# Kernel optimization log

Measured on AMD Instinct MI355X. Metric: run time of the kernel, lower is better.

## Reference

```python
import jax, jax.numpy as jnp
import numpy as np

B, C, D = 8, 512, 128

def setup_inputs() -> dict:
    key = jax.random.key(0)
    k1, k2, k3 = jax.random.split(key, 3)
    queries = jax.random.normal(k1, (B, C, D), dtype=jnp.float32)
    keys = jax.random.normal(k2, (B, C, D), dtype=jnp.float32)
    # docstring says keys are L2-normalized
    keys = keys / jnp.linalg.norm(keys, axis=-1, keepdims=True)
    carry_over = jax.random.normal(k3, (D, D), dtype=jnp.float32) * 0.1
    return {"queries": queries, "keys": keys, "carry_over": carry_over}

def reference(queries, keys, carry_over):
    # per-position outer products: (B, C, D, D)
    outer = jnp.einsum('bci,bcj->bcij', keys, keys)
    # causal prefix-sum state + carried-over state from previous chunk
    proj = jnp.cumsum(outer, axis=1) + carry_over[None, None, :, :]
    # apply state to queries: out_i = sum_j proj[b,c,i,j] * q[b,c,j]
    projected_queries = jnp.einsum('bcij,bcj->bci', proj, queries)
    # new carry: batch-mean of final-position state
    new_carry_over = jnp.mean(proj[:, -1], axis=0)
    return projected_queries, new_carry_over
```

## Files before the change

### kernel.cpp

```cpp
#include <hip/hip_runtime.h>

#define B_ 8
#define C_ 512
#define D_ 128
#define LDK 136
#define LDT 40

typedef __bf16 v8bf __attribute__((ext_vector_type(8)));
typedef float v4f __attribute__((ext_vector_type(4)));
typedef float fvec4 __attribute__((ext_vector_type(4)));
typedef unsigned short u16;
typedef u16 u16x4 __attribute__((ext_vector_type(4)));

__device__ __forceinline__ u16 f2bf(float f) {
  unsigned u = __builtin_bit_cast(unsigned, f);
  u = u + 0x7FFFu + ((u >> 16) & 1u);
  return (u16)(u >> 16);
}

__global__ __launch_bounds__(256) void k_gram(const float* __restrict__ K,
                                              float* __restrict__ G) {
  const int t = blockIdx.x, b = blockIdx.y;
  const int tid = threadIdx.x;
  const int w = tid >> 6, l = tid & 63, lr = l & 15, lg = l >> 4;
  const float* Kc = K + (size_t)(b * C_ + t * 32) * D_;

  v8bf fr[8];
#pragma unroll
  for (int n = 0; n < 8; ++n) {
    u16 tmp[8];
#pragma unroll
    for (int e = 0; e < 8; ++e)
      tmp[e] = f2bf(Kc[(size_t)(8 * lg + e) * D_ + 16 * n + lr]);
    fr[n] = *(const v8bf*)tmp;
  }
  float* Gp = G + (size_t)(b * 16 + t) * 16384;
#pragma unroll
  for (int mi = 0; mi < 2; ++mi) {
    v8bf am = fr[2 * w + mi];
#pragma unroll
    for (int n = 0; n < 8; ++n) {
      v4f z = {0.f, 0.f, 0.f, 0.f};
      v4f a = __builtin_amdgcn_mfma_f32_16x16x32_bf16(am, fr[n], z, 0, 0, 0);
#pragma unroll
      for (int j = 0; j < 4; ++j)
        Gp[(size_t)(32 * w + 16 * mi + 4 * lg + j) * 128 + 16 * n + lr] = a[j];
    }
  }
}

__global__ __launch_bounds__(256) void k_prefix(const float* __restrict__ G,
                                                const float* __restrict__ carry,
                                                u16* __restrict__ Mp,
                                                float* __restrict__ tot) {
  const int b = blockIdx.y;
  const int e = blockIdx.x * 256 + threadIdx.x;
  const float c = carry[e];
  const float* gb = G + (size_t)b * 16 * 16384 + e;
  u16* mb = Mp + (size_t)b * 16 * 16384 + e;
  float run = 0.f;
#pragma unroll
  for (int t = 0; t < 16; ++t) {
    float g = gb[(size_t)t * 16384];
    mb[(size_t)t * 16384] = f2bf(c + run);
    run += g;
  }
  tot[(size_t)b * 16384 + e] = run;
}

__global__ __launch_bounds__(256) void k_out(
    const float* __restrict__ Q, const float* __restrict__ K,
    const u16* __restrict__ Mp, const float* __restrict__ tot,
    const float* __restrict__ carry, float* __restrict__ out,
    float* __restrict__ out2) {
  const int t = blockIdx.x, b = blockIdx.y;
  const int tid = threadIdx.x;

  if (t == 16) {
    const int e0 = b * 2048 + tid * 8;
    fvec4 s0 = {0.f, 0.f, 0.f, 0.f}, s1 = {0.f, 0.f, 0.f, 0.f};
#pragma unroll
    for (int bb = 0; bb < 8; ++bb) {
      s0 += *(const fvec4*)(tot + (size_t)bb * 16384 + e0);
      s1 += *(const fvec4*)(tot + (size_t)bb * 16384 + e0 + 4);
    }
    fvec4 c0 = *(const fvec4*)(carry + e0);
    fvec4 c1 = *(const fvec4*)(carry + e0 + 4);
    *(fvec4*)(out2 + e0) = c0 + 0.125f * s0;
    *(fvec4*)(out2 + e0 + 4) = c1 + 0.125f * s1;
    return;
  }

  const int w = tid >> 6, l = tid & 63, lr = l & 15, lg = l >> 4;
  const int wr = (w & 1) * 16, wc = (w >> 1) * 64, sc0 = (w >> 1) * 16;
  const int r0 = t * 32;

  __shared__ u16 sl[32 * 40];

  const float* Kc = K + (size_t)(b * C_ + r0) * D_;

  v8bf pb[4];
#pragma unroll
  for (int n = 0; n < 4; ++n) {
    u16 tmp[8];
#pragma unroll
    for (int e = 0; e < 8; ++e)
      tmp[e] = f2bf(Kc[(size_t)(8 * lg + e) * D_ + wc + 16 * n + lr]);
    pb[n] = *(const v8bf*)tmp;
  }

  v8bf sb[4];
  {
    const float* krow = Kc + (size_t)(sc0 + lr) * D_;
#pragma unroll
    for (int kk = 0; kk < 4; ++kk) {
      fvec4 a = *(const fvec4*)(krow + kk * 32 + 8 * lg);
      fvec4 c2 = *(const fvec4*)(krow + kk * 32 + 8 * lg + 4);
      u16 tmp[8] = {f2bf(a[0]),  f2bf(a[1]),  f2bf(a[2]),  f2bf(a[3]),
                    f2bf(c2[0]), f2bf(c2[1]), f2bf(c2[2]), f2bf(c2[3])};
      sb[kk] = *(const v8bf*)tmp;
    }
  }

  v8bf qf[4];
  {
    const float* qrow = Q + (size_t)(b * C_ + r0 + wr + lr) * D_;
#pragma unroll
    for (int kk = 0; kk < 4; ++kk) {
      const float* p = qrow + kk * 32 + 8 * lg;
      fvec4 a = *(const fvec4*)p;
      fvec4 c2 = *(const fvec4*)(p + 4);
      u16 tmp[8] = {f2bf(a[0]),  f2bf(a[1]),  f2bf(a[2]),  f2bf(a[3]),
                    f2bf(c2[0]), f2bf(c2[1]), f2bf(c2[2]), f2bf(c2[3])};
      qf[kk] = *(const v8bf*)tmp;
    }
  }

  v8bf mf[4][4];
  {
    const u16* mp = Mp + (size_t)(b * 16 + t) * 16384;
#pragma unroll
    for (int kk = 0; kk < 4; ++kk)
#pragma unroll
      for (int n = 0; n < 4; ++n)
        mf[kk][n] =
            *(const v8bf*)(mp + (size_t)(wc + 16 * n + lr) * 128 + 32 * kk +
                           8 * lg);
  }

  v4f sacc = {0.f, 0.f, 0.f, 0.f};
#pragma unroll
  for (int kk = 0; kk < 4; ++kk)
    sacc = __builtin_amdgcn_mfma_f32_16x16x32_bf16(qf[kk], sb[kk], sacc, 0, 0, 0);
#pragma unroll
  for (int j = 0; j < 4; ++j) {
    const int sr = wr + lg * 4 + j;
    const int sc = sc0 + lr;
    float v = sacc[j];
    if (sc > sr) v = 0.f;
    sl[sr * 40 + sc] = f2bf(v);
  }

  v4f acc[4] = {{0.f, 0.f, 0.f, 0.f}, {0.f, 0.f, 0.f, 0.f},
                {0.f, 0.f, 0.f, 0.f}, {0.f, 0.f, 0.f, 0.f}};
#pragma unroll
  for (int kk = 0; kk < 4; ++kk)
#pragma unroll
    for (int n = 0; n < 4; ++n)
      acc[n] = __builtin_amdgcn_mfma_f32_16x16x32_bf16(qf[kk], mf[kk][n],
                                                       acc[n], 0, 0, 0);
  __syncthreads();

  v8bf af = *(const v8bf*)&sl[(wr + lr) * 40 + lg * 8];
#pragma unroll
  for (int n = 0; n < 4; ++n)
    acc[n] = __builtin_amdgcn_mfma_f32_16x16x32_bf16(af, pb[n], acc[n], 0, 0, 0);

#pragma unroll
  for (int n = 0; n < 4; ++n)
#pragma unroll
    for (int j = 0; j < 4; ++j)
      out[(size_t)(b * C_ + r0 + wr + lg * 4 + j) * D_ + wc + n * 16 + lr] =
          acc[n][j];
}

__device__ __forceinline__ int kt_idx(int d, int r) {
  return d * LDT + ((((r >> 3) ^ ((d >> 2) & 3))) << 3) + (r & 7);
}
__device__ __forceinline__ v8bf kt_frag(const u16* ktb, int col, int lg) {
  return *(const v8bf*)&ktb[col * LDT + (((lg ^ ((col >> 2) & 3))) << 3)];
}
__device__ __forceinline__ void load_chunk(const float* __restrict__ Kbase,
                                           int tid, fvec4* pf) {
#pragma unroll
  for (int i = 0; i < 4; ++i)
    pf[i] = *(const fvec4*)(Kbase + i * 1024 + tid * 4);
}
__device__ __forceinline__ void write_stage(const fvec4* pf, u16* ksb, u16* ktb,
                                            int tid) {
  const int d0 = (tid & 31) * 4;
  const int rb = tid >> 5;
#pragma unroll
  for (int i = 0; i < 4; ++i) {
    const int r = i * 8 + rb;
    fvec4 v = pf[i];
    u16 h0 = f2bf(v[0]), h1 = f2bf(v[1]), h2 = f2bf(v[2]), h3 = f2bf(v[3]);
    u16x4 u = {h0, h1, h2, h3};
    *(u16x4*)&ksb[r * LDK + d0] = u;
    ktb[kt_idx(d0 + 0, r)] = h0;
    ktb[kt_idx(d0 + 1, r)] = h1;
    ktb[kt_idx(d0 + 2, r)] = h2;
    ktb[kt_idx(d0 + 3, r)] = h3;
  }
}

__global__ __launch_bounds__(256) void k_proj_fb(
    const float* __restrict__ Q, const float* __restrict__ K,
    const float* __restrict__ carry, float* __restrict__ out) {
  const int t = blockIdx.x, b = blockIdx.y;
  const int tid = threadIdx.x;
  const int w = tid >> 6, l = tid & 63, lr = l & 15, lg = l >> 4;
  const int wr = (w & 1) * 16, wc = (w >> 1) * 64;
  const int r0 = t * 32;

  __shared__ u16 ks[2][32 * LDK];
  __shared__ u16 kt[2][128 * LDT];
  __shared__ u16 sl[32 * 40];

  const float* Kb0 = K + (size_t)(b * C_) * D_;
  fvec4 pf[4];
  load_chunk(Kb0, tid, pf);

  v8bf qf[4];
  {
    const float* qrow = Q + (size_t)(b * C_ + r0 + wr + lr) * D_;
#pragma unroll
    for (int kk = 0; kk < 4; ++kk) {
      const float* p = qrow + kk * 32 + lg * 8;
      fvec4 a = *(const fvec4*)p;
      fvec4 c2 = *(const fvec4*)(p + 4);
      u16 tmp[8] = {f2bf(a[0]),  f2bf(a[1]),  f2bf(a[2]),  f2bf(a[3]),
                    f2bf(c2[0]), f2bf(c2[1]), f2bf(c2[2]), f2bf(c2[3])};
      qf[kk] = *(const v8bf*)tmp;
    }
  }

  v4f acc[4] = {{0.f, 0.f, 0.f, 0.f}, {0.f, 0.f, 0.f, 0.f},
                {0.f, 0.f, 0.f, 0.f}, {0.f, 0.f, 0.f, 0.f}};
#pragma unroll
  for (int kk = 0; kk < 4; ++kk) {
#pragma unroll
    for (int n = 0; n < 4; ++n) {
      const float* p =
          carry + (size_t)(wc + n * 16 + lr) * D_ + kk * 32 + lg * 8;
      fvec4 a = *(const fvec4*)p;
      fvec4 c2 = *(const fvec4*)(p + 4);
      u16 tmp[8] = {f2bf(a[0]),  f2bf(a[1]),  f2bf(a[2]),  f2bf(a[3]),
                    f2bf(c2[0]), f2bf(c2[1]), f2bf(c2[2]), f2bf(c2[3])};
      acc[n] = __builtin_amdgcn_mfma_f32_16x16x32_bf16(
          qf[kk], *(const v8bf*)tmp, acc[n], 0, 0, 0);
    }
  }

  write_stage(pf, ks[0], kt[0], tid);
  __syncthreads();

  int cur = 0;
  const int sc0 = (w >> 1) * 16;
  for (int cc = 0; cc <= t; ++cc) {
    const bool more = (cc < t);
    fvec4 nf[4];
    if (more) load_chunk(Kb0 + (size_t)(cc + 1) * 32 * D_, tid, nf);

    v4f sacc = {0.f, 0.f, 0.f, 0.f};
#pragma unroll
    for (int kk = 0; kk < 4; ++kk) {
      v8bf bf = *(const v8bf*)&ks[cur][(sc0 + lr) * LDK + kk * 32 + lg * 8];
      sacc = __builtin_amdgcn_mfma_f32_16x16x32_bf16(qf[kk], bf, sacc, 0, 0, 0);
    }
    const bool diag = (cc == t);
#pragma unroll
    for (int j = 0; j < 4; ++j) {
      const int sr = wr + lg * 4 + j;
      const int sc = sc0 + lr;
      float v = sacc[j];
      if (diag && sc > sr) v = 0.f;
      sl[sr * 40 + sc] = f2bf(v);
    }
    __syncthreads();

    v8bf af = *(const v8bf*)&sl[(wr + lr) * 40 + lg * 8];
#pragma unroll
    for (int n = 0; n < 4; ++n) {
      v8bf bf = kt_frag(kt[cur], wc + n * 16 + lr, lg);
      acc[n] = __builtin_amdgcn_mfma_f32_16x16x32_bf16(af, bf, acc[n], 0, 0, 0);
    }
    if (more) {
      write_stage(nf, ks[cur ^ 1], kt[cur ^ 1], tid);
      cur ^= 1;
    }
    __syncthreads();
  }

#pragma unroll
  for (int n = 0; n < 4; ++n)
#pragma unroll
    for (int j = 0; j < 4; ++j)
      out[(size_t)(b * C_ + r0 + wr + lg * 4 + j) * D_ + wc + n * 16 + lr] =
          acc[n][j];
}

__global__ __launch_bounds__(256) void k_syrk_direct(
    const float* __restrict__ K, const float* __restrict__ carry,
    float* __restrict__ out2) {
  const int tid = threadIdx.x;
  const int w = tid >> 6, l = tid & 63, lr = l & 15, lg = l >> 4;
  __shared__ u16 kt[2][128 * LDT];

  v4f acc[2][8];
#pragma unroll
  for (int mi = 0; mi < 2; ++mi)
#pragma unroll
    for (int n = 0; n < 8; ++n) acc[mi][n] = (v4f){0.f, 0.f, 0.f, 0.f};

  fvec4 pf[4];
  load_chunk(K, tid, pf);
  {
    const int d0 = (tid & 31) * 4;
    const int rb = tid >> 5;
#pragma unroll
    for (int i = 0; i < 4; ++i) {
      const int r = i * 8 + rb;
      fvec4 v = pf[i];
      kt[0][kt_idx(d0 + 0, r)] = f2bf(v[0]);
      kt[0][kt_idx(d0 + 1, r)] = f2bf(v[1]);
      kt[0][kt_idx(d0 + 2, r)] = f2bf(v[2]);
      kt[0][kt_idx(d0 + 3, r)] = f2bf(v[3]);
    }
  }
  __syncthreads();
  int cur = 0;
  for (int g = 0; g < 128; ++g) {
    const bool more = (g < 127);
    fvec4 nf[4];
    if (more) load_chunk(K + (size_t)(g + 1) * 32 * D_, tid, nf);
    v8bf fr[8];
#pragma unroll
    for (int x = 0; x < 8; ++x) fr[x] = kt_frag(kt[cur], x * 16 + lr, lg);
#pragma unroll
    for (int mi = 0; mi < 2; ++mi)
#pragma unroll
      for (int n = 0; n < 8; ++n)
        acc[mi][n] = __builtin_amdgcn_mfma_f32_16x16x32_bf16(
            fr[2 * w + mi], fr[n], acc[mi][n], 0, 0, 0);
    if (more) {
      const int d0 = (tid & 31) * 4;
      const int rb = tid >> 5;
      u16* kb = kt[cur ^ 1];
#pragma unroll
      for (int i = 0; i < 4; ++i) {
        const int r = i * 8 + rb;
        fvec4 v = nf[i];
        kb[kt_idx(d0 + 0, r)] = f2bf(v[0]);
        kb[kt_idx(d0 + 1, r)] = f2bf(v[1]);
        kb[kt_idx(d0 + 2, r)] = f2bf(v[2]);
        kb[kt_idx(d0 + 3, r)] = f2bf(v[3]);
      }
      cur ^= 1;
    }
    __syncthreads();
  }
#pragma unroll
  for (int mi = 0; mi < 2; ++mi)
#pragma unroll
    for (int n = 0; n < 8; ++n)
#pragma unroll
      for (int j = 0; j < 4; ++j) {
        const int idx = (16 * (2 * w + mi) + 4 * lg + j) * 128 + 16 * n + lr;
        out2[idx] = carry[idx] + 0.125f * acc[mi][n][j];
      }
}

extern "C" void kernel_launch(void* const* d_in, const int* in_sizes, int n_in,
                              void* d_out, int out_size, void* d_ws,
                              size_t ws_size, hipStream_t stream) {
  const float* Q = (const float*)d_in[0];
  const float* K = (const float*)d_in[1];
  const float* carry = (const float*)d_in[2];
  float* out = (float*)d_out;
  float* out2 = out + (size_t)B_ * C_ * D_;

  const size_t nG = (size_t)128 * 16384;
  const size_t nMpF = nG / 2;
  const size_t need = (nG + nMpF + (size_t)8 * 16384) * sizeof(float);

  if (ws_size >= need) {
    float* G = (float*)d_ws;
    u16* Mp = (u16*)((float*)d_ws + nG);
    float* tot = (float*)d_ws + nG + nMpF;
    k_gram<<<dim3(16, 8), 256, 0, stream>>>(K, G);
    k_prefix<<<dim3(64, 8), 256, 0, stream>>>(G, carry, Mp, tot);
    k_out<<<dim3(17, 8), 256, 0, stream>>>(Q, K, Mp, tot, carry, out, out2);
  } else {
    k_proj_fb<<<dim3(16, 8), 256, 0, stream>>>(Q, K, carry, out);
    k_syrk_direct<<<1, 256, 0, stream>>>(K, carry, out2);
  }
}
```

Baseline: 27.85 us.

## Drop prefix-scan kernel; accumulate prior chunk Grams directly in output kernel

Removes the separate k_prefix kernel. k_gram now stores per-chunk Gram matrices in bf16, and each k_out block loops over all earlier chunks' Grams with MFMA instead of reading a precomputed prefix state. The carry contribution is applied by converting carry to bf16 on the fly, and the new-carry block sums all 128 bf16 Grams itself. This saves one launch and the fp32 G round trip, but adds load imbalance (later chunks do up to 15x more MFMA work), a serial 128-step reduction in one block, and extra bf16 rounding error on the per-chunk sums.

Result: slower. 67.54 us (+142.5%).

```diff
diff --git a/kernel.cpp b/kernel.cpp
--- a/kernel.cpp
+++ b/kernel.cpp
@@ -11,15 +11,20 @@
 typedef float fvec4 __attribute__((ext_vector_type(4)));
 typedef unsigned short u16;
 typedef u16 u16x4 __attribute__((ext_vector_type(4)));
+typedef u16 u16x8 __attribute__((ext_vector_type(8)));
 
 __device__ __forceinline__ u16 f2bf(float f) {
   unsigned u = __builtin_bit_cast(unsigned, f);
   u = u + 0x7FFFu + ((u >> 16) & 1u);
   return (u16)(u >> 16);
 }
+__device__ __forceinline__ float bf2f(u16 h) {
+  unsigned u = ((unsigned)h) << 16;
+  return __builtin_bit_cast(float, u);
+}
 
 __global__ __launch_bounds__(256) void k_gram(const float* __restrict__ K,
-                                              float* __restrict__ G) {
+                                              u16* __restrict__ G) {
   const int t = blockIdx.x, b = blockIdx.y;
   const int tid = threadIdx.x;
   const int w = tid >> 6, l = tid & 63, lr = l & 15, lg = l >> 4;
@@ -34,7 +39,7 @@
       tmp[e] = f2bf(Kc[(size_t)(8 * lg + e) * D_ + 16 * n + lr]);
     fr[n] = *(const v8bf*)tmp;
   }
-  float* Gp = G + (size_t)(b * 16 + t) * 16384;
+  u16* Gp = G + (size_t)(b * 16 + t) * 16384;
 #pragma unroll
   for (int mi = 0; mi < 2; ++mi) {
     v8bf am = fr[2 * w + mi];
@@ -44,50 +49,30 @@
       v4f a = __builtin_amdgcn_mfma_f32_16x16x32_bf16(am, fr[n], z, 0, 0, 0);
 #pragma unroll
       for (int j = 0; j < 4; ++j)
-        Gp[(size_t)(32 * w + 16 * mi + 4 * lg + j) * 128 + 16 * n + lr] = a[j];
-    }
-  }
-}
-
-__global__ __launch_bounds__(256) void k_prefix(const float* __restrict__ G,
-                                                const float* __restrict__ carry,
-                                                u16* __restrict__ Mp,
-                                                float* __restrict__ tot) {
-  const int b = blockIdx.y;
-  const int e = blockIdx.x * 256 + threadIdx.x;
-  const float c = carry[e];
-  const float* gb = G + (size_t)b * 16 * 16384 + e;
-  u16* mb = Mp + (size_t)b * 16 * 16384 + e;
-  float run = 0.f;
-#pragma unroll
-  for (int t = 0; t < 16; ++t) {
-    float g = gb[(size_t)t * 16384];
-    mb[(size_t)t * 16384] = f2bf(c + run);
-    run += g;
-  }
-  tot[(size_t)b * 16384 + e] = run;
+        Gp[(size_t)(32 * w + 16 * mi + 4 * lg + j) * 128 + 16 * n + lr] =
+            f2bf(a[j]);
+    }
+  }
 }
 
 __global__ __launch_bounds__(256) void k_out(
     const float* __restrict__ Q, const float* __restrict__ K,
-    const u16* __restrict__ Mp, const float* __restrict__ tot,
-    const float* __restrict__ carry, float* __restrict__ out,
-    float* __restrict__ out2) {
+    const u16* __restrict__ G, const float* __restrict__ carry,
+    float* __restrict__ out, float* __restrict__ out2) {
   const int t = blockIdx.x, b = blockIdx.y;
   const int tid = threadIdx.x;
 
   if (t == 16) {
     const int e0 = b * 2048 + tid * 8;
-    fvec4 s0 = {0.f, 0.f, 0.f, 0.f}, s1 = {0.f, 0.f, 0.f, 0.f};
-#pragma unroll
-    for (int bb = 0; bb < 8; ++bb) {
-      s0 += *(const fvec4*)(tot + (size_t)bb * 16384 + e0);
-      s1 += *(const fvec4*)(tot + (size_t)bb * 16384 + e0 + 4);
-    }
-    fvec4 c0 = *(const fvec4*)(carry + e0);
-    fvec4 c1 = *(const fvec4*)(carry + e0 + 4);
-    *(fvec4*)(out2 + e0) = c0 + 0.125f * s0;
-    *(fvec4*)(out2 + e0 + 4) = c1 + 0.125f * s1;
+    float s[8] = {0.f, 0.f, 0.f, 0.f, 0.f, 0.f, 0.f, 0.f};
+    for (int p = 0; p < 128; ++p) {
+      u16x8 g = *(const u16x8*)(G + (size_t)p * 16384 + e0);
+#pragma unroll
+      for (int i = 0; i < 8; ++i) s[i] += bf2f(g[i]);
+    }
+#pragma unroll
+    for (int i = 0; i < 8; ++i)
+      out2[e0 + i] = carry[e0 + i] + 0.125f * s[i];
     return;
   }
 
@@ -136,22 +121,11 @@
     }
   }
 
-  v8bf mf[4][4];
-  {
-    const u16* mp = Mp + (size_t)(b * 16 + t) * 16384;
-#pragma unroll
-    for (int kk = 0; kk < 4; ++kk)
-#pragma unroll
-      for (int n = 0; n < 4; ++n)
-        mf[kk][n] =
-            *(const v8bf*)(mp + (size_t)(wc + 16 * n + lr) * 128 + 32 * kk +
-                           8 * lg);
-  }
-
   v4f sacc = {0.f, 0.f, 0.f, 0.f};
 #pragma unroll
   for (int kk = 0; kk < 4; ++kk)
-    sacc = __builtin_amdgcn_mfma_f32_16x16x32_bf16(qf[kk], sb[kk], sacc, 0, 0, 0);
+    sacc =
+        __builtin_amdgcn_mfma_f32_16x16x32_bf16(qf[kk], sb[kk], sacc, 0, 0, 0);
 #pragma unroll
   for (int j = 0; j < 4; ++j) {
     const int sr = wr + lg * 4 + j;
@@ -164,17 +138,41 @@
   v4f acc[4] = {{0.f, 0.f, 0.f, 0.f}, {0.f, 0.f, 0.f, 0.f},
                 {0.f, 0.f, 0.f, 0.f}, {0.f, 0.f, 0.f, 0.f}};
 #pragma unroll
-  for (int kk = 0; kk < 4; ++kk)
-#pragma unroll
-    for (int n = 0; n < 4; ++n)
-      acc[n] = __builtin_amdgcn_mfma_f32_16x16x32_bf16(qf[kk], mf[kk][n],
-                                                       acc[n], 0, 0, 0);
+  for (int kk = 0; kk < 4; ++kk) {
+#pragma unroll
+    for (int n = 0; n < 4; ++n) {
+      const float* p =
+          carry + (size_t)(wc + 16 * n + lr) * D_ + 32 * kk + 8 * lg;
+      fvec4 a = *(const fvec4*)p;
+      fvec4 c2 = *(const fvec4*)(p + 4);
+      u16 tmp[8] = {f2bf(a[0]),  f2bf(a[1]),  f2bf(a[2]),  f2bf(a[3]),
+                    f2bf(c2[0]), f2bf(c2[1]), f2bf(c2[2]), f2bf(c2[3])};
+      acc[n] = __builtin_amdgcn_mfma_f32_16x16x32_bf16(
+          qf[kk], *(const v8bf*)tmp, acc[n], 0, 0, 0);
+    }
+  }
+
+  const u16* Gb = G + (size_t)(b * 16) * 16384;
+  for (int tp = 0; tp < t; ++tp) {
+    const u16* gp = Gb + (size_t)tp * 16384;
+#pragma unroll
+    for (int kk = 0; kk < 4; ++kk) {
+#pragma unroll
+      for (int n = 0; n < 4; ++n) {
+        v8bf mf = *(const v8bf*)(gp + (size_t)(wc + 16 * n + lr) * 128 +
+                                 32 * kk + 8 * lg);
+        acc[n] = __builtin_amdgcn_mfma_f32_16x16x32_bf16(qf[kk], mf, acc[n],
+                                                         0, 0, 0);
+      }
+    }
+  }
   __syncthreads();
 
   v8bf af = *(const v8bf*)&sl[(wr + lr) * 40 + lg * 8];
 #pragma unroll
   for (int n = 0; n < 4; ++n)
-    acc[n] = __builtin_amdgcn_mfma_f32_16x16x32_bf16(af, pb[n], acc[n], 0, 0, 0);
+    acc[n] =
+        __builtin_amdgcn_mfma_f32_16x16x32_bf16(af, pb[n], acc[n], 0, 0, 0);
 
 #pragma unroll
   for (int n = 0; n < 4; ++n)
@@ -390,17 +388,12 @@
   float* out = (float*)d_out;
   float* out2 = out + (size_t)B_ * C_ * D_;
 
-  const size_t nG = (size_t)128 * 16384;
-  const size_t nMpF = nG / 2;
-  const size_t need = (nG + nMpF + (size_t)8 * 16384) * sizeof(float);
+  const size_t need = (size_t)128 * 16384 * sizeof(u16);
 
   if (ws_size >= need) {
-    float* G = (float*)d_ws;
-    u16* Mp = (u16*)((float*)d_ws + nG);
-    float* tot = (float*)d_ws + nG + nMpF;
+    u16* G = (u16*)d_ws;
     k_gram<<<dim3(16, 8), 256, 0, stream>>>(K, G);
-    k_prefix<<<dim3(64, 8), 256, 0, stream>>>(G, carry, Mp, tot);
-    k_out<<<dim3(17, 8), 256, 0, stream>>>(Q, K, Mp, tot, carry, out, out2);
+    k_out<<<dim3(17, 8), 256, 0, stream>>>(Q, K, G, carry, out, out2);
   } else {
     k_proj_fb<<<dim3(16, 8), 256, 0, stream>>>(Q, K, carry, out);
     k_syrk_direct<<<1, 256, 0, stream>>>(K, carry, out2);
```

## Store per-chunk Gram matrices in bf16 and stage K tiles through LDS

Applied to the files above, without the earlier changes.

The per-chunk Gram matrices are now written in bf16 instead of fp32, which halves the workspace traffic between the gram and prefix kernels. The prefix kernel processes eight elements per thread with vector loads and stores and launches far fewer blocks. The gram and output kernels now load K with coalesced vector reads into LDS and build MFMA fragments from there, replacing strided scalar global loads. The trade-off is extra bf16 rounding in the prefix-sum accumulation, which may reduce accuracy of the carried state.

After: 26.74 us. 4.0% less time.

```diff
diff --git a/kernel.cpp b/kernel.cpp
--- a/kernel.cpp
+++ b/kernel.cpp
@@ -3,6 +3,8 @@
 #define B_ 8
 #define C_ 512
 #define D_ 128
+#define LDG 132
+#define LDO 136
 #define LDK 136
 #define LDT 40
 
@@ -11,30 +13,60 @@
 typedef float fvec4 __attribute__((ext_vector_type(4)));
 typedef unsigned short u16;
 typedef u16 u16x4 __attribute__((ext_vector_type(4)));
+typedef u16 u16x8 __attribute__((ext_vector_type(8)));
 
 __device__ __forceinline__ u16 f2bf(float f) {
   unsigned u = __builtin_bit_cast(unsigned, f);
   u = u + 0x7FFFu + ((u >> 16) & 1u);
   return (u16)(u >> 16);
 }
-
-__global__ __launch_bounds__(256) void k_gram(const float* __restrict__ K,
-                                              float* __restrict__ G) {
+__device__ __forceinline__ float bf2f(u16 h) {
+  unsigned u = ((unsigned)h) << 16;
+  return __builtin_bit_cast(float, u);
+}
+
+__device__ __forceinline__ void load_chunk(const float* __restrict__ Kbase,
+                                           int tid, fvec4* pf) {
+#pragma unroll
+  for (int i = 0; i < 4; ++i)
+    pf[i] = *(const fvec4*)(Kbase + i * 1024 + tid * 4);
+}
+
+template <int STRIDE>
+__device__ __forceinline__ void lds_put(const fvec4* pf, u16* ksb, int tid) {
+  const int d0 = (tid & 31) * 4;
+  const int rb = tid >> 5;
+#pragma unroll
+  for (int i = 0; i < 4; ++i) {
+    const int r = i * 8 + rb;
+    fvec4 v = pf[i];
+    u16x4 u = {f2bf(v[0]), f2bf(v[1]), f2bf(v[2]), f2bf(v[3])};
+    *(u16x4*)&ksb[r * STRIDE + d0] = u;
+  }
+}
+
+__global__ __launch_bounds__(256, 1) void k_gram(const float* __restrict__ K,
+                                                 u16* __restrict__ G) {
   const int t = blockIdx.x, b = blockIdx.y;
   const int tid = threadIdx.x;
   const int w = tid >> 6, l = tid & 63, lr = l & 15, lg = l >> 4;
-  const float* Kc = K + (size_t)(b * C_ + t * 32) * D_;
+
+  __shared__ u16 ks[32 * LDG];
+
+  fvec4 pf[4];
+  load_chunk(K + (size_t)(b * C_ + t * 32) * D_, tid, pf);
+  lds_put<LDG>(pf, ks, tid);
+  __syncthreads();
 
   v8bf fr[8];
 #pragma unroll
   for (int n = 0; n < 8; ++n) {
     u16 tmp[8];
 #pragma unroll
-    for (int e = 0; e < 8; ++e)
-      tmp[e] = f2bf(Kc[(size_t)(8 * lg + e) * D_ + 16 * n + lr]);
+    for (int e = 0; e < 8; ++e) tmp[e] = ks[(8 * lg + e) * LDG + 16 * n + lr];
     fr[n] = *(const v8bf*)tmp;
   }
-  float* Gp = G + (size_t)(b * 16 + t) * 16384;
+  u16* Gp = G + (size_t)(b * 16 + t) * 16384;
 #pragma unroll
   for (int mi = 0; mi < 2; ++mi) {
     v8bf am = fr[2 * w + mi];
@@ -44,31 +76,40 @@
       v4f a = __builtin_amdgcn_mfma_f32_16x16x32_bf16(am, fr[n], z, 0, 0, 0);
 #pragma unroll
       for (int j = 0; j < 4; ++j)
-        Gp[(size_t)(32 * w + 16 * mi + 4 * lg + j) * 128 + 16 * n + lr] = a[j];
-    }
-  }
-}
-
-__global__ __launch_bounds__(256) void k_prefix(const float* __restrict__ G,
-                                                const float* __restrict__ carry,
-                                                u16* __restrict__ Mp,
-                                                float* __restrict__ tot) {
+        Gp[(size_t)(32 * w + 16 * mi + 4 * lg + j) * 128 + 16 * n + lr] =
+            f2bf(a[j]);
+    }
+  }
+}
+
+__global__ __launch_bounds__(256, 1) void k_prefix(
+    const u16* __restrict__ G, const float* __restrict__ carry,
+    u16* __restrict__ Mp, float* __restrict__ tot) {
   const int b = blockIdx.y;
-  const int e = blockIdx.x * 256 + threadIdx.x;
-  const float c = carry[e];
-  const float* gb = G + (size_t)b * 16 * 16384 + e;
-  u16* mb = Mp + (size_t)b * 16 * 16384 + e;
-  float run = 0.f;
+  const int e0 = blockIdx.x * 2048 + threadIdx.x * 8;
+  fvec4 c0 = *(const fvec4*)(carry + e0);
+  fvec4 c1 = *(const fvec4*)(carry + e0 + 4);
+  float c[8] = {c0[0], c0[1], c0[2], c0[3], c1[0], c1[1], c1[2], c1[3]};
+  float run[8] = {0.f, 0.f, 0.f, 0.f, 0.f, 0.f, 0.f, 0.f};
+  const u16* gb = G + (size_t)b * 16 * 16384 + e0;
+  u16* mb = Mp + (size_t)b * 16 * 16384 + e0;
 #pragma unroll
   for (int t = 0; t < 16; ++t) {
-    float g = gb[(size_t)t * 16384];
-    mb[(size_t)t * 16384] = f2bf(c + run);
-    run += g;
-  }
-  tot[(size_t)b * 16384 + e] = run;
-}
-
-__global__ __launch_bounds__(256) void k_out(
+    u16x8 g = *(const u16x8*)(gb + (size_t)t * 16384);
+    u16x8 m;
+#pragma unroll
+    for (int i = 0; i < 8; ++i) m[i] = f2bf(c[i] + run[i]);
+    *(u16x8*)(mb + (size_t)t * 16384) = m;
+#pragma unroll
+    for (int i = 0; i < 8; ++i) run[i] += bf2f(g[i]);
+  }
+  fvec4 r0 = {run[0], run[1], run[2], run[3]};
+  fvec4 r1 = {run[4], run[5], run[6], run[7]};
+  *(fvec4*)(tot + (size_t)b * 16384 + e0) = r0;
+  *(fvec4*)(tot + (size_t)b * 16384 + e0 + 4) = r1;
+}
+
+__global__ __launch_bounds__(256, 1) void k_out(
     const float* __restrict__ Q, const float* __restrict__ K,
     const u16* __restrict__ Mp, const float* __restrict__ tot,
     const float* __restrict__ carry, float* __restrict__ out,
@@ -95,32 +136,11 @@
   const int wr = (w & 1) * 16, wc = (w >> 1) * 64, sc0 = (w >> 1) * 16;
   const int r0 = t * 32;
 
+  __shared__ u16 ks[32 * LDO];
   __shared__ u16 sl[32 * 40];
 
-  const float* Kc = K + (size_t)(b * C_ + r0) * D_;
-
-  v8bf pb[4];
-#pragma unroll
-  for (int n = 0; n < 4; ++n) {
-    u16 tmp[8];
-#pragma unroll
-    for (int e = 0; e < 8; ++e)
-      tmp[e] = f2bf(Kc[(size_t)(8 * lg + e) * D_ + wc + 16 * n + lr]);
-    pb[n] = *(const v8bf*)tmp;
-  }
-
-  v8bf sb[4];
-  {
-    const float* krow = Kc + (size_t)(sc0 + lr) * D_;
-#pragma unroll
-    for (int kk = 0; kk < 4; ++kk) {
-      fvec4 a = *(const fvec4*)(krow + kk * 32 + 8 * lg);
-      fvec4 c2 = *(const fvec4*)(krow + kk * 32 + 8 * lg + 4);
-      u16 tmp[8] = {f2bf(a[0]),  f2bf(a[1]),  f2bf(a[2]),  f2bf(a[3]),
-                    f2bf(c2[0]), f2bf(c2[1]), f2bf(c2[2]), f2bf(c2[3])};
-      sb[kk] = *(const v8bf*)tmp;
-    }
-  }
+  fvec4 pf[4];
+  load_chunk(K + (size_t)(b * C_ + r0) * D_, tid, pf);
 
   v8bf qf[4];
   {
@@ -143,15 +163,33 @@
     for (int kk = 0; kk < 4; ++kk)
 #pragma unroll
       for (int n = 0; n < 4; ++n)
-        mf[kk][n] =
-            *(const v8bf*)(mp + (size_t)(wc + 16 * n + lr) * 128 + 32 * kk +
-                           8 * lg);
+        mf[kk][n] = *(const v8bf*)(mp + (size_t)(wc + 16 * n + lr) * 128 +
+                                   32 * kk + 8 * lg);
+  }
+
+  lds_put<LDO>(pf, ks, tid);
+  __syncthreads();
+
+  v8bf sb[4];
+#pragma unroll
+  for (int kk = 0; kk < 4; ++kk)
+    sb[kk] = *(const v8bf*)&ks[(sc0 + lr) * LDO + 32 * kk + 8 * lg];
+
+  v8bf pb[4];
+#pragma unroll
+  for (int n = 0; n < 4; ++n) {
+    u16 tmp[8];
+#pragma unroll
+    for (int e = 0; e < 8; ++e)
+      tmp[e] = ks[(8 * lg + e) * LDO + wc + 16 * n + lr];
+    pb[n] = *(const v8bf*)tmp;
   }
 
   v4f sacc = {0.f, 0.f, 0.f, 0.f};
 #pragma unroll
   for (int kk = 0; kk < 4; ++kk)
-    sacc = __builtin_amdgcn_mfma_f32_16x16x32_bf16(qf[kk], sb[kk], sacc, 0, 0, 0);
+    sacc =
+        __builtin_amdgcn_mfma_f32_16x16x32_bf16(qf[kk], sb[kk], sacc, 0, 0, 0);
 #pragma unroll
   for (int j = 0; j < 4; ++j) {
     const int sr = wr + lg * 4 + j;
@@ -174,7 +212,8 @@
   v8bf af = *(const v8bf*)&sl[(wr + lr) * 40 + lg * 8];
 #pragma unroll
   for (int n = 0; n < 4; ++n)
-    acc[n] = __builtin_amdgcn_mfma_f32_16x16x32_bf16(af, pb[n], acc[n], 0, 0, 0);
+    acc[n] =
+        __builtin_amdgcn_mfma_f32_16x16x32_bf16(af, pb[n], acc[n], 0, 0, 0);
 
 #pragma unroll
   for (int n = 0; n < 4; ++n)
@@ -189,12 +228,6 @@
 }
 __device__ __forceinline__ v8bf kt_frag(const u16* ktb, int col, int lg) {
   return *(const v8bf*)&ktb[col * LDT + (((lg ^ ((col >> 2) & 3))) << 3)];
-}
-__device__ __forceinline__ void load_chunk(const float* __restrict__ Kbase,
-                                           int tid, fvec4* pf) {
-#pragma unroll
-  for (int i = 0; i < 4; ++i)
-    pf[i] = *(const fvec4*)(Kbase + i * 1024 + tid * 4);
 }
 __device__ __forceinline__ void write_stage(const fvec4* pf, u16* ksb, u16* ktb,
                                             int tid) {
@@ -390,16 +423,15 @@
   float* out = (float*)d_out;
   float* out2 = out + (size_t)B_ * C_ * D_;
 
-  const size_t nG = (size_t)128 * 16384;
-  const size_t nMpF = nG / 2;
-  const size_t need = (nG + nMpF + (size_t)8 * 16384) * sizeof(float);
+  const size_t nGu = (size_t)128 * 16384;
+  const size_t need = nGu * 2 * sizeof(u16) + (size_t)8 * 16384 * sizeof(float);
 
   if (ws_size >= need) {
-    float* G = (float*)d_ws;
-    u16* Mp = (u16*)((float*)d_ws + nG);
-    float* tot = (float*)d_ws + nG + nMpF;
+    u16* G = (u16*)d_ws;
+    u16* Mp = G + nGu;
+    float* tot = (float*)(Mp + nGu);
     k_gram<<<dim3(16, 8), 256, 0, stream>>>(K, G);
-    k_prefix<<<dim3(64, 8), 256, 0, stream>>>(G, carry, Mp, tot);
+    k_prefix<<<dim3(8, 8), 256, 0, stream>>>(G, carry, Mp, tot);
     k_out<<<dim3(17, 8), 256, 0, stream>>>(Q, K, Mp, tot, carry, out, out2);
   } else {
     k_proj_fb<<<dim3(16, 8), 256, 0, stream>>>(Q, K, carry, out);
```
